# Kernel tuning notes

Hardware: AMD Instinct MI355X
Metric: run time of the kernel (lower is better)

The kernel has to match this reference:

```python
import jax, jax.numpy as jnp
import numpy as np

B, S, D, H = 2, 2048, 1024, 16
HD = D // H
LN_EPS = 1e-5


def setup_inputs() -> dict:
    key = jax.random.key(0)
    ks = jax.random.split(key, 8)
    inv = 1.0 / np.sqrt(D)
    return {
        "embedded": jax.random.normal(ks[0], (B, S, D), dtype=jnp.float32),
        "Wq": jax.random.normal(ks[1], (D, D), dtype=jnp.float32) * inv,
        "bq": jax.random.normal(ks[2], (D,), dtype=jnp.float32) * 0.01,
        "Wk": jax.random.normal(ks[3], (D, D), dtype=jnp.float32) * inv,
        "bk": jax.random.normal(ks[4], (D,), dtype=jnp.float32) * 0.01,
        "Wv": jax.random.normal(ks[5], (D, D), dtype=jnp.float32) * inv,
        "bv": jax.random.normal(ks[6], (D,), dtype=jnp.float32) * 0.01,
        "gamma": jnp.ones((D,), dtype=jnp.float32),
        "beta": jnp.zeros((D,), dtype=jnp.float32),
    }


def reference(embedded, Wq, bq, Wk, bk, Wv, bv, gamma, beta):
    b, s, d = embedded.shape
    # QKV projections (torch Linear: x @ W^T + b)
    q = embedded @ Wq.T + bq
    k = embedded @ Wk.T + bk
    v = embedded @ Wv.T + bv
    # [b, s, H, hd] -> [b, H, s, hd]
    q = q.reshape(b, s, H, HD).transpose(0, 2, 1, 3)
    k = k.reshape(b, s, H, HD).transpose(0, 2, 1, 3)
    v = v.reshape(b, s, H, HD).transpose(0, 2, 1, 3)
    # scores [b, H, s, s]
    qk = jnp.einsum("bhqd,bhkd->bhqk", q, k)
    # NaN scrub -> -inf (original: qk[qk != qk] = -inf)
    qk = jnp.where(jnp.isnan(qk), -jnp.inf, qk)
    # NOTE: original scales by sqrt(shape[-1]) == sqrt(seq_len), not head_dim
    qk = qk / jnp.float32(np.sqrt(s))
    p = jax.nn.softmax(qk, axis=-1)
    p = jnp.where(jnp.isnan(p), 0.0, p)
    v = jnp.where(jnp.isnan(v), 0.0, v)
    # post-softmax upper-triangular (incl. diagonal) mask, no renormalization
    mask = jnp.triu(jnp.ones((s, s), dtype=p.dtype), k=0)
    p = p * mask
    z = jnp.einsum("bhqk,bhkd->bhqd", p, v)  # [b, H, s, hd]
    # original does a raw .view(b, s, -1) on contiguous [b,h,s,hd] (no transpose)
    z = z.reshape(b, s, d)
    # residual + LayerNorm
    x = embedded + z
    mu = jnp.mean(x, axis=-1, keepdims=True)
    var = jnp.mean(jnp.square(x - mu), axis=-1, keepdims=True)
    out = (x - mu) * jax.lax.rsqrt(var + LN_EPS) * gamma + beta
    return out
```

## Files before the change

### kernel.cpp

```cpp
#include <hip/hip_runtime.h>
#include <hip/hip_bf16.h>
#include <math.h>

typedef unsigned short ushort_t;
typedef unsigned char uchar_t;
typedef __attribute__((ext_vector_type(8))) short short8;
typedef __attribute__((ext_vector_type(4))) float f32x4;

struct __align__(8) us4 { ushort_t u[4]; };

__device__ __forceinline__ ushort_t f2bf(float x) {
  union { float f; unsigned u; } c; c.f = x;
  unsigned r = c.u + 0x7FFFu + ((c.u >> 16) & 1u);
  return (ushort_t)(r >> 16);
}
__device__ __forceinline__ float bf2f(ushort_t b) {
  union { unsigned u; float f; } c; c.u = ((unsigned)b) << 16;
  return c.f;
}

#define CEXP_SCALE (0.02209708691f * 1.44269504089f)

struct CvtArgs { const float* s[4]; ushort_t* d[4]; };

__global__ __launch_bounds__(256) void cvt_all(CvtArgs c) {
  int bid = blockIdx.x;
  int job, base;
  if (bid < 4096) { job = 0; base = bid; }
  else { job = 1 + ((bid - 4096) >> 10); base = (bid - 4096) & 1023; }
  int i = (base * 256 + threadIdx.x) * 4;
  f32x4 v = *(const f32x4*)(c.s[job] + i);
  us4 o;
  o.u[0] = f2bf(v[0]); o.u[1] = f2bf(v[1]); o.u[2] = f2bf(v[2]); o.u[3] = f2bf(v[3]);
  *(us4*)(c.d[job] + i) = o;
}

struct QkvArgs {
  const ushort_t* X;
  const ushort_t* W0; const ushort_t* W1; const ushort_t* W2;
  const float* b0; const float* b1; const float* b2;
  ushort_t* o0; ushort_t* o1;
  uchar_t* vt;
};

__global__ __launch_bounds__(256) void qkv_gemm(QkvArgs a) {
  __shared__ __align__(16) ushort_t As[128 * 64];
  __shared__ __align__(16) ushort_t Bs[128 * 64];
  const int z = blockIdx.z;
  const ushort_t* W  = (z == 0) ? a.W0 : ((z == 1) ? a.W1 : a.W2);
  const float* bias  = (z == 0) ? a.b0 : ((z == 1) ? a.b1 : a.b2);
  const int mBase = blockIdx.x * 128;
  const int nBase = blockIdx.y * 128;
  const int tid  = threadIdx.x;
  const int lane = tid & 63;
  const int w    = tid >> 6;
  const int wm   = w >> 1, wn = w & 1;
  const int quad = lane >> 4;
  const int l15  = lane & 15;
  const int l7   = l15 & 7;

  f32x4 acc[4][4] = {};

  const int srow = lane >> 3;
  const int scol = ((lane & 7) ^ srow) * 8;
  const ushort_t* gA0 = a.X + (mBase + srow) * 1024 + scol;
  const ushort_t* gB0 = W   + (nBase + srow) * 1024 + scol;

  for (int k0 = 0; k0 < 1024; k0 += 64) {
#pragma unroll
    for (int p = 0; p < 4; ++p) {
      int j = w * 4 + p;
      __builtin_amdgcn_global_load_lds(
          (const __attribute__((address_space(1))) void*)(gA0 + j * 8 * 1024 + k0),
          (__attribute__((address_space(3))) void*)(As + j * 512), 16, 0, 0);
      __builtin_amdgcn_global_load_lds(
          (const __attribute__((address_space(1))) void*)(gB0 + j * 8 * 1024 + k0),
          (__attribute__((address_space(3))) void*)(Bs + j * 512), 16, 0, 0);
    }
    __syncthreads();
    short8 af[2][4], bfr[2][4];
#pragma unroll
    for (int kk = 0; kk < 2; ++kk) {
#pragma unroll
      for (int mi = 0; mi < 4; ++mi)
        af[kk][mi] = *(const short8*)(As + (wm * 64 + mi * 16 + l15) * 64 + (((kk * 4 + quad) ^ l7) * 8));
#pragma unroll
      for (int ni = 0; ni < 4; ++ni)
        bfr[kk][ni] = *(const short8*)(Bs + (wn * 64 + ni * 16 + l15) * 64 + (((kk * 4 + quad) ^ l7) * 8));
    }
#pragma unroll
    for (int kk = 0; kk < 2; ++kk)
#pragma unroll
      for (int mi = 0; mi < 4; ++mi)
#pragma unroll
        for (int ni = 0; ni < 4; ++ni)
          acc[mi][ni] = __builtin_amdgcn_mfma_f32_16x16x32_bf16(af[kk][mi], bfr[kk][ni], acc[mi][ni], 0, 0, 0);
    __syncthreads();
  }

  if (z == 2) {
#pragma unroll
    for (int ni = 0; ni < 4; ++ni) {
      int n = nBase + wn * 64 + ni * 16 + l15;
      float bv = bias[n];
      int h = n >> 6, hd = n & 63;
#pragma unroll
      for (int mi = 0; mi < 4; ++mi) {
        int m0 = mBase + wm * 64 + mi * 16 + quad * 4;
        int bb = m0 >> 11, s = m0 & 2047;
        float x0 = acc[mi][ni][0] + bv, x1 = acc[mi][ni][1] + bv;
        float x2 = acc[mi][ni][2] + bv, x3 = acc[mi][ni][3] + bv;
        unsigned int pk = __builtin_amdgcn_cvt_pk_fp8_f32(x0, x1, 0, false);
        pk = __builtin_amdgcn_cvt_pk_fp8_f32(x2, x3, pk, true);
        int dest = (s & ~127) + ((((s >> 4) & 7) ^ (hd & 7)) * 16) + (s & 15);
        *(unsigned int*)(a.vt + (size_t)(bb * 16 + h) * 131072 + (size_t)hd * 2048 + dest) = pk;
      }
    }
  } else {
    ushort_t* out = (z == 0) ? a.o0 : a.o1;
    const int swz = (z == 1) ? 7 : 0;
    const float osc = (z == 0) ? CEXP_SCALE : 1.0f;
#pragma unroll
    for (int ni = 0; ni < 4; ++ni) {
      int n = nBase + wn * 64 + ni * 16 + l15;
      float bv = bias[n];
      int h = n >> 6, hd = n & 63;
      int hdHi = hd >> 3, hdLo = hd & 7;
#pragma unroll
      for (int mi = 0; mi < 4; ++mi) {
        int m0 = mBase + wm * 64 + mi * 16 + quad * 4;
#pragma unroll
        for (int r = 0; r < 4; ++r) {
          int m = m0 + r;
          int bb = m >> 11, s = m & 2047;
          int hdw = (((hdHi ^ (s & swz)) << 3) | hdLo);
          out[((bb * 16 + h) * 2048 + s) * 64 + hdw] = f2bf((acc[mi][ni][r] + bv) * osc);
        }
      }
    }
  }
}

__global__ __launch_bounds__(256) void attn_kernel(const ushort_t* __restrict__ qb,
                                                   const ushort_t* __restrict__ kb,
                                                   const uchar_t* __restrict__ vT,
                                                   ushort_t* __restrict__ zb) {
  __shared__ __align__(16) ushort_t Ks[128 * 64];
  __shared__ __align__(16) uchar_t  Vt[64 * 128];
  __shared__ __align__(16) uchar_t  Ps[128 * 128];
  const int n_lin = blockIdx.x + 16 * blockIdx.y;
  const int xcd = n_lin & 7;
  const int j   = n_lin >> 3;
  const int hi  = (j >> 5) & 1;
  const int xb  = (j >> 2) & 7;
  const int xq  = hi ? (15 - xb) : xb;
  const int bh  = xcd * 4 + (j & 3);

  const int qblk = xq * 128;
  const int tid  = threadIdx.x;
  const int lane = tid & 63;
  const int w    = tid >> 6;
  const int quad = lane >> 4;
  const int l15  = lane & 15;
  const int l7   = l15 & 7;

  const ushort_t* qpage = qb + (size_t)bh * (2048 * 64);
  const ushort_t* kpage = kb + (size_t)bh * (2048 * 64);
  const uchar_t*  vpage = vT + (size_t)bh * (64 * 2048);

  short8 qf[2][2];
#pragma unroll
  for (int nb = 0; nb < 2; ++nb) {
    int qg = qblk + w * 32 + nb * 16 + l15;
#pragma unroll
    for (int kd = 0; kd < 2; ++kd)
      qf[nb][kd] = *(const short8*)(qpage + (size_t)qg * 64 + kd * 32 + quad * 8);
  }

  float psum[2] = {0.f, 0.f};
  f32x4 o[4][2] = {};

  for (int kt = 0; kt < 2048; kt += 128) {
    const bool needP    = (kt >= qblk);
    const bool boundary = (kt == qblk);
    __syncthreads();

#pragma unroll
    for (int p = 0; p < 4; ++p) {
      int jj = w * 4 + p;
      __builtin_amdgcn_global_load_lds(
          (const __attribute__((address_space(1))) void*)(kpage + (size_t)kt * 64 + jj * 512 + lane * 8),
          (__attribute__((address_space(3))) void*)(Ks + jj * 512), 16, 0, 0);
    }
    if (needP) {
#pragma unroll
      for (int p = 0; p < 2; ++p) {
        int jj = w * 2 + p;
        __builtin_amdgcn_global_load_lds(
            (const __attribute__((address_space(1))) void*)(vpage + (size_t)(jj * 8 + (lane >> 3)) * 2048 + kt + (lane & 7) * 16),
            (__attribute__((address_space(3))) void*)(Vt + jj * 1024), 16, 0, 0);
      }
    }
    __syncthreads();

#pragma unroll
    for (int mb = 0; mb < 8; ++mb) {
      const ushort_t* krow = Ks + (mb * 16 + l15) * 64;
      short8 kf0 = *(const short8*)(krow + ((0 + quad) ^ l7) * 8);
      short8 kf1 = *(const short8*)(krow + ((4 + quad) ^ l7) * 8);
      f32x4 s0 = {}, s1 = {};
      s0 = __builtin_amdgcn_mfma_f32_16x16x32_bf16(kf0, qf[0][0], s0, 0, 0, 0);
      s0 = __builtin_amdgcn_mfma_f32_16x16x32_bf16(kf1, qf[0][1], s0, 0, 0, 0);
      s1 = __builtin_amdgcn_mfma_f32_16x16x32_bf16(kf0, qf[1][0], s1, 0, 0, 0);
      s1 = __builtin_amdgcn_mfma_f32_16x16x32_bf16(kf1, qf[1][1], s1, 0, 0, 0);
      const int keyb = kt + mb * 16 + quad * 4;
#pragma unroll
      for (int nb = 0; nb < 2; ++nb) {
        f32x4 s = nb ? s1 : s0;
        float p0 = __builtin_amdgcn_exp2f(s[0]);
        float p1 = __builtin_amdgcn_exp2f(s[1]);
        float p2 = __builtin_amdgcn_exp2f(s[2]);
        float p3 = __builtin_amdgcn_exp2f(s[3]);
        psum[nb] += (p0 + p1) + (p2 + p3);
        if (needP) {
          unsigned int pk;
          if (boundary) {
            int qg = qblk + w * 32 + nb * 16 + l15;
            float m0 = (keyb + 0 >= qg) ? p0 : 0.f;
            float m1 = (keyb + 1 >= qg) ? p1 : 0.f;
            float m2 = (keyb + 2 >= qg) ? p2 : 0.f;
            float m3 = (keyb + 3 >= qg) ? p3 : 0.f;
            pk = __builtin_amdgcn_cvt_pk_fp8_f32(m0, m1, 0, false);
            pk = __builtin_amdgcn_cvt_pk_fp8_f32(m2, m3, pk, true);
          } else {
            pk = __builtin_amdgcn_cvt_pk_fp8_f32(p0, p1, 0, false);
            pk = __builtin_amdgcn_cvt_pk_fp8_f32(p2, p3, pk, true);
          }
          *(unsigned int*)(Ps + (w * 32 + nb * 16 + l15) * 128 + ((mb ^ l7) * 16) + quad * 4) = pk;
        }
      }
    }

    if (needP) {
#pragma unroll
      for (int kd = 0; kd < 4; ++kd) {
        const int un = ((kd * 2 + (quad >> 1)) ^ l7) * 16 + (quad & 1) * 8;
        long long pf0 = *(const long long*)(Ps + (w * 32 + l15) * 128 + un);
        long long pf1 = *(const long long*)(Ps + (w * 32 + 16 + l15) * 128 + un);
#pragma unroll
        for (int mb = 0; mb < 4; ++mb) {
          long long vf = *(const long long*)(Vt + (mb * 16 + l15) * 128 + un);
          o[mb][0] = __builtin_amdgcn_mfma_f32_16x16x32_fp8_fp8(vf, pf0, o[mb][0], 0, 0, 0);
          o[mb][1] = __builtin_amdgcn_mfma_f32_16x16x32_fp8_fp8(vf, pf1, o[mb][1], 0, 0, 0);
        }
      }
    }
  }

#pragma unroll
  for (int nb = 0; nb < 2; ++nb) {
    psum[nb] += __shfl_xor(psum[nb], 16, 64);
    psum[nb] += __shfl_xor(psum[nb], 32, 64);
    float rl = 1.0f / psum[nb];
    int qg = qblk + w * 32 + nb * 16 + l15;
#pragma unroll
    for (int mb = 0; mb < 4; ++mb)
#pragma unroll
      for (int r = 0; r < 4; ++r) {
        int hd = mb * 16 + quad * 4 + r;
        zb[((size_t)bh * 2048 + qg) * 64 + hd] = f2bf(o[mb][nb][r] * rl);
      }
  }
}

__global__ __launch_bounds__(256) void ln_kernel(const float* __restrict__ emb,
                                                 const ushort_t* __restrict__ zb,
                                                 const float* __restrict__ gamma,
                                                 const float* __restrict__ beta,
                                                 float* __restrict__ out) {
  __shared__ float red[2][4];
  int row = blockIdx.x;
  int b = row >> 11, s = row & 2047;
  int h = s >> 7;
  int siHi = (s & 127) << 4;
  int tid = threadIdx.x;
  int dcol = tid * 4;
  int si = siHi | (dcol >> 6);
  int j = dcol & 63;

  f32x4 e4 = *(const f32x4*)(emb + (size_t)row * 1024 + dcol);
  us4 z4 = *(const us4*)(zb + (((size_t)(b * 16 + h) * 2048 + si) * 64 + j));
  float x0 = e4[0] + bf2f(z4.u[0]);
  float x1 = e4[1] + bf2f(z4.u[1]);
  float x2 = e4[2] + bf2f(z4.u[2]);
  float x3 = e4[3] + bf2f(z4.u[3]);

  float sum = x0 + x1 + x2 + x3;
  float sq  = x0 * x0 + x1 * x1 + x2 * x2 + x3 * x3;
#pragma unroll
  for (int off = 1; off <= 32; off <<= 1) {
    sum += __shfl_xor(sum, off, 64);
    sq  += __shfl_xor(sq,  off, 64);
  }
  int wv = tid >> 6;
  if ((tid & 63) == 0) { red[0][wv] = sum; red[1][wv] = sq; }
  __syncthreads();
  float ts = red[0][0] + red[0][1] + red[0][2] + red[0][3];
  float tq = red[1][0] + red[1][1] + red[1][2] + red[1][3];
  float mu = ts * (1.0f / 1024.0f);
  float var = tq * (1.0f / 1024.0f) - mu * mu;
  float rsig = rsqrtf(var + 1e-5f);

  f32x4 g4 = *(const f32x4*)(gamma + dcol);
  f32x4 b4 = *(const f32x4*)(beta + dcol);
  f32x4 o4;
  o4[0] = (x0 - mu) * rsig * g4[0] + b4[0];
  o4[1] = (x1 - mu) * rsig * g4[1] + b4[1];
  o4[2] = (x2 - mu) * rsig * g4[2] + b4[2];
  o4[3] = (x3 - mu) * rsig * g4[3] + b4[3];
  *(f32x4*)(out + (size_t)row * 1024 + dcol) = o4;
}

extern "C" void kernel_launch(void* const* d_in, const int* in_sizes, int n_in,
                              void* d_out, int out_size, void* d_ws, size_t ws_size,
                              hipStream_t stream) {
  (void)in_sizes; (void)n_in; (void)out_size; (void)ws_size;
  const float* emb   = (const float*)d_in[0];
  const float* Wq    = (const float*)d_in[1];
  const float* bq    = (const float*)d_in[2];
  const float* Wk    = (const float*)d_in[3];
  const float* bk    = (const float*)d_in[4];
  const float* Wv    = (const float*)d_in[5];
  const float* bv    = (const float*)d_in[6];
  const float* gamma = (const float*)d_in[7];
  const float* beta  = (const float*)d_in[8];
  float* out = (float*)d_out;

  char* ws = (char*)d_ws;
  ushort_t* Xbf  = (ushort_t*)(ws);
  ushort_t* Wqb  = (ushort_t*)(ws + 8388608);
  ushort_t* Wkb  = (ushort_t*)(ws + 10485760);
  ushort_t* Wvb  = (ushort_t*)(ws + 12582912);
  ushort_t* qbuf = (ushort_t*)(ws + 14680064);
  ushort_t* kbuf = (ushort_t*)(ws + 23068672);
  ushort_t* zbuf = (ushort_t*)(ws + 31457280);
  uchar_t*  vTb  = (uchar_t*)(ws + 39845888);

  CvtArgs c;
  c.s[0] = emb; c.s[1] = Wq; c.s[2] = Wk; c.s[3] = Wv;
  c.d[0] = Xbf; c.d[1] = Wqb; c.d[2] = Wkb; c.d[3] = Wvb;
  cvt_all<<<7168, 256, 0, stream>>>(c);

  QkvArgs a;
  a.X = Xbf;
  a.W0 = Wqb; a.W1 = Wkb; a.W2 = Wvb;
  a.b0 = bq;  a.b1 = bk;  a.b2 = bv;
  a.o0 = qbuf; a.o1 = kbuf;
  a.vt = vTb;
  qkv_gemm<<<dim3(32, 8, 3), 256, 0, stream>>>(a);

  attn_kernel<<<dim3(16, 32), 256, 0, stream>>>(qbuf, kbuf, vTb, zbuf);

  ln_kernel<<<4096, 256, 0, stream>>>(emb, zbuf, gamma, beta, out);
}
```

Baseline: 182.7 us.

## Split attention key range across two blocks and reduce partials

```diff
diff --git a/kernel.cpp b/kernel.cpp
--- a/kernel.cpp
+++ b/kernel.cpp
@@ -144,7 +144,10 @@
 __global__ __launch_bounds__(256) void attn_kernel(const ushort_t* __restrict__ qb,
                                                    const ushort_t* __restrict__ kb,
                                                    const uchar_t* __restrict__ vT,
-                                                   ushort_t* __restrict__ zb) {
+                                                   ushort_t* __restrict__ oA,
+                                                   ushort_t* __restrict__ oB,
+                                                   float* __restrict__ pA,
+                                                   float* __restrict__ pB) {
   __shared__ __align__(16) ushort_t Ks[128 * 64];
   __shared__ __align__(16) uchar_t  Vt[64 * 128];
   __shared__ __align__(16) uchar_t  Ps[128 * 128];
@@ -156,6 +159,11 @@
   const int xq  = hi ? (15 - xb) : xb;
   const int bh  = xcd * 4 + (j & 3);
 
+  const int half = blockIdx.z;
+  ushort_t* oPart = half ? oB : oA;
+  float*    pPart = half ? pB : pA;
+  const int ktLo = half << 10;
+
   const int qblk = xq * 128;
   const int tid  = threadIdx.x;
   const int lane = tid & 63;
@@ -180,7 +188,7 @@
   float psum[2] = {0.f, 0.f};
   f32x4 o[4][2] = {};
 
-  for (int kt = 0; kt < 2048; kt += 128) {
+  for (int kt = ktLo; kt < ktLo + 1024; kt += 128) {
     const bool needP    = (kt >= qblk);
     const bool boundary = (kt == qblk);
     __syncthreads();
@@ -261,16 +269,33 @@
   for (int nb = 0; nb < 2; ++nb) {
     psum[nb] += __shfl_xor(psum[nb], 16, 64);
     psum[nb] += __shfl_xor(psum[nb], 32, 64);
-    float rl = 1.0f / psum[nb];
     int qg = qblk + w * 32 + nb * 16 + l15;
+    if (quad == 0)
+      pPart[(size_t)bh * 2048 + qg] = psum[nb];
 #pragma unroll
     for (int mb = 0; mb < 4; ++mb)
 #pragma unroll
       for (int r = 0; r < 4; ++r) {
         int hd = mb * 16 + quad * 4 + r;
-        zb[((size_t)bh * 2048 + qg) * 64 + hd] = f2bf(o[mb][nb][r] * rl);
-      }
-  }
+        oPart[((size_t)bh * 2048 + qg) * 64 + hd] = f2bf(o[mb][nb][r]);
+      }
+  }
+}
+
+__global__ __launch_bounds__(256) void red_kernel(ushort_t* __restrict__ oA,
+                                                  const ushort_t* __restrict__ oB,
+                                                  const float* __restrict__ pA,
+                                                  const float* __restrict__ pB) {
+  int t = blockIdx.x * 256 + threadIdx.x;
+  int row = t >> 3;
+  float rl = 1.0f / (pA[row] + pB[row]);
+  short8 a = *(const short8*)(oA + (size_t)t * 8);
+  short8 b = *(const short8*)(oB + (size_t)t * 8);
+  short8 o;
+#pragma unroll
+  for (int i = 0; i < 8; ++i)
+    o[i] = (short)f2bf((bf2f((ushort_t)a[i]) + bf2f((ushort_t)b[i])) * rl);
+  *(short8*)(oA + (size_t)t * 8) = o;
 }
 
 __global__ __launch_bounds__(256) void ln_kernel(const float* __restrict__ emb,
@@ -343,8 +368,12 @@
   ushort_t* Wvb  = (ushort_t*)(ws + 12582912);
   ushort_t* qbuf = (ushort_t*)(ws + 14680064);
   ushort_t* kbuf = (ushort_t*)(ws + 23068672);
-  ushort_t* zbuf = (ushort_t*)(ws + 31457280);
   uchar_t*  vTb  = (uchar_t*)(ws + 39845888);
+
+  ushort_t* oA = (ushort_t*)(ws);
+  float*    pA = (float*)(ws + 8388608);
+  float*    pB = (float*)(ws + 8650752);
+  ushort_t* oB = (ushort_t*)(ws + 31457280);
 
   CvtArgs c;
   c.s[0] = emb; c.s[1] = Wq; c.s[2] = Wk; c.s[3] = Wv;
@@ -359,7 +388,9 @@
   a.vt = vTb;
   qkv_gemm<<<dim3(32, 8, 3), 256, 0, stream>>>(a);
 
-  attn_kernel<<<dim3(16, 32), 256, 0, stream>>>(qbuf, kbuf, vTb, zbuf);
-
-  ln_kernel<<<4096, 256, 0, stream>>>(emb, zbuf, gamma, beta, out);
-}
+  attn_kernel<<<dim3(16, 32, 2), 256, 0, stream>>>(qbuf, kbuf, vTb, oA, oB, pA, pB);
+
+  red_kernel<<<2048, 256, 0, stream>>>(oA, oB, pA, pB);
+
+  ln_kernel<<<4096, 256, 0, stream>>>(emb, oA, gamma, beta, out);
+}
```

After: 191.2 us. 1.05x slower.
